# Kernel tuning notes

Measured on AMD Instinct MI355X. Metric: run time of the kernel, lower is better.

The kernel has to match this reference:

```python
import jax, jax.numpy as jnp
import numpy as np

D_MODEL = 128
N_HEADS = 8
HEAD_DIM = D_MODEL // N_HEADS
N_NODES = 50000
N_EDGES = 640000


def setup_inputs() -> dict:
    key = jax.random.key(0)
    ks = jax.random.split(key, 10)
    sd = 1.0 / np.sqrt(D_MODEL)
    return {
        "node_embeds": jax.random.normal(ks[0], (N_NODES, D_MODEL), dtype=jnp.float32),
        "edge_index": jax.random.randint(ks[1], (2, N_EDGES), 0, N_NODES, dtype=jnp.int64),
        "Wq": jax.random.uniform(ks[2], (D_MODEL, D_MODEL), jnp.float32, -sd, sd),
        "bq": jax.random.uniform(ks[3], (D_MODEL,), jnp.float32, -sd, sd),
        "Wk": jax.random.uniform(ks[4], (D_MODEL, D_MODEL), jnp.float32, -sd, sd),
        "bk": jax.random.uniform(ks[5], (D_MODEL,), jnp.float32, -sd, sd),
        "Wv": jax.random.uniform(ks[6], (D_MODEL, D_MODEL), jnp.float32, -sd, sd),
        "bv": jax.random.uniform(ks[7], (D_MODEL,), jnp.float32, -sd, sd),
        "gamma": jnp.ones((D_MODEL,), jnp.float32),
        "beta": jnp.zeros((D_MODEL,), jnp.float32),
    }


def reference(node_embeds, edge_index, Wq, bq, Wk, bk, Wv, bv, gamma, beta):
    num_nodes = node_embeds.shape[0]
    rows, cols = edge_index[0], edge_index[1]
    src = node_embeds[rows]  # (E, d)
    tgt = node_embeds[cols]  # (E, d)
    q = (src @ Wq.T + bq).reshape(-1, N_HEADS, HEAD_DIM)
    k = (tgt @ Wk.T + bk).reshape(-1, N_HEADS, HEAD_DIM)
    v = (tgt @ Wv.T + bv).reshape(-1, N_HEADS, HEAD_DIM)
    att = jnp.einsum('ehd,ehd->eh', q, k) / jnp.sqrt(jnp.float32(HEAD_DIM))
    exp_att = jnp.exp(jnp.clip(att, -10.0, 10.0))  # (E, h)
    att_sum = jax.ops.segment_sum(exp_att, rows, num_segments=num_nodes)  # (N, h)
    att_norm = exp_att / (att_sum[rows] + 1e-8)
    weighted_v = (att_norm[..., None] * v).reshape(-1, D_MODEL)  # (E, d)
    out = jax.ops.segment_sum(weighted_v, rows, num_segments=num_nodes)
    out = out + node_embeds
    # LayerNorm, eps=1e-6
    mu = jnp.mean(out, axis=-1, keepdims=True)
    var = jnp.mean(jnp.square(out - mu), axis=-1, keepdims=True)
    out = (out - mu) * jax.lax.rsqrt(var + 1e-6) * gamma + beta
    return out
```

## Files before the change

### kernel.cpp

```cpp
#include <hip/hip_runtime.h>
#include <hip/hip_bf16.h>
#include <cstdint>

#define D_MODEL 128
#define N_HEADS 8
#define HEAD_DIM 16

typedef __attribute__((ext_vector_type(8))) short bf16x8;
typedef __attribute__((ext_vector_type(4))) float f32x4;

static __device__ __forceinline__ float b2f(unsigned short u) {
  unsigned int x = ((unsigned int)u) << 16;
  return __builtin_bit_cast(float, x);
}
static __device__ __forceinline__ unsigned short f2b(float f) {
  __hip_bfloat16 h = __float2bfloat16(f);
  return __builtin_bit_cast(unsigned short, h);
}

__global__ __launch_bounds__(256) void hist_qkv_kernel(
    const int* __restrict__ rows, int* __restrict__ cnt, int E,
    const float* __restrict__ X,
    const float* __restrict__ Wq, const float* __restrict__ Wk,
    const float* __restrict__ Wv,
    const float* __restrict__ bq, const float* __restrict__ bk,
    const float* __restrict__ bv,
    unsigned short* __restrict__ Qo, unsigned short* __restrict__ Ko,
    unsigned short* __restrict__ Vo, int N, int nbQ)
{
  __shared__ unsigned short Wl[128 * 128];

  if ((int)blockIdx.x >= nbQ) {
    const int e = (blockIdx.x - nbQ) * 256 + threadIdx.x;
    if (e < E) atomicAdd(&cnt[rows[e]], 1);
    return;
  }

  const int t    = threadIdx.x;
  const int wave = t >> 6;
  const int l    = t & 63;
  const int lr   = l & 15;
  const int lg   = l >> 4;
  const int nw   = blockIdx.x * 128 + wave * 32;

  bf16x8 a[2][4];
  #pragma unroll
  for (int ng = 0; ng < 2; ++ng) {
    const int arow = nw + ng * 16 + lr;
    if (arow < N) {
      const float* xp = X + (size_t)arow * D_MODEL + lg * 8;
      #pragma unroll
      for (int ks = 0; ks < 4; ++ks) {
        const float4 f0 = reinterpret_cast<const float4*>(xp + ks * 32)[0];
        const float4 f1 = reinterpret_cast<const float4*>(xp + ks * 32)[1];
        unsigned short tm[8];
        tm[0] = f2b(f0.x); tm[1] = f2b(f0.y); tm[2] = f2b(f0.z); tm[3] = f2b(f0.w);
        tm[4] = f2b(f1.x); tm[5] = f2b(f1.y); tm[6] = f2b(f1.z); tm[7] = f2b(f1.w);
        a[ng][ks] = *reinterpret_cast<bf16x8*>(tm);
      }
    } else {
      #pragma unroll
      for (int ks = 0; ks < 4; ++ks) a[ng][ks] = bf16x8{0,0,0,0,0,0,0,0};
    }
  }

  const float* wmats[3]  = {Wq, Wk, Wv};
  const float* biases[3] = {bq, bk, bv};
  unsigned short* outs[3] = {Qo, Ko, Vo};

  #pragma unroll 1
  for (int m = 0; m < 3; ++m) {
    __syncthreads();
    {
      const float* __restrict__ wsrc = wmats[m];
      uint4* wl4 = reinterpret_cast<uint4*>(Wl);
      #pragma unroll
      for (int i = 0; i < 8; ++i) {
        const int cg = i * 256 + t;
        const int r  = cg >> 4;
        const int j  = cg & 15;
        const float4 f0 = reinterpret_cast<const float4*>(wsrc + cg * 8)[0];
        const float4 f1 = reinterpret_cast<const float4*>(wsrc + cg * 8)[1];
        unsigned short tm[8];
        tm[0] = f2b(f0.x); tm[1] = f2b(f0.y); tm[2] = f2b(f0.z); tm[3] = f2b(f0.w);
        tm[4] = f2b(f1.x); tm[5] = f2b(f1.y); tm[6] = f2b(f1.z); tm[7] = f2b(f1.w);
        wl4[r * 16 + (j ^ (r & 7))] = *reinterpret_cast<uint4*>(tm);
      }
    }
    __syncthreads();

    unsigned short* __restrict__ O = outs[m];
    const float* __restrict__ bias = biases[m];
    float bias8[8];
    #pragma unroll
    for (int c = 0; c < 8; ++c) bias8[c] = bias[c * 16 + lr];

    #pragma unroll
    for (int c = 0; c < 8; ++c) {
      const int row = c * 16 + lr;
      bf16x8 w[4];
      #pragma unroll
      for (int ks = 0; ks < 4; ++ks) {
        const int j = ks * 4 + lg;
        w[ks] = *reinterpret_cast<const bf16x8*>(
            Wl + ((row * 16 + (j ^ (row & 7))) * 8));
      }
      #pragma unroll
      for (int ng = 0; ng < 2; ++ng) {
        f32x4 acc = {bias8[c], bias8[c], bias8[c], bias8[c]};
        #pragma unroll
        for (int ks = 0; ks < 4; ++ks)
          acc = __builtin_amdgcn_mfma_f32_16x16x32_bf16(a[ng][ks], w[ks], acc, 0, 0, 0);
        #pragma unroll
        for (int r = 0; r < 4; ++r) {
          const int orow = nw + ng * 16 + lg * 4 + r;
          if (orow < N) O[(size_t)orow * D_MODEL + c * 16 + lr] = f2b(acc[r]);
        }
      }
    }
  }
}

__global__ __launch_bounds__(256) void emit_kernel(
    const int* __restrict__ cnt, int* __restrict__ row_ptr,
    int* __restrict__ row_cur, int N, int E)
{
  __shared__ int red[4];
  __shared__ int psum[256];
  __shared__ int base_s;
  const int b = blockIdx.x;
  const int t = threadIdx.x;

  int s = 0;
  {
    const int npre4 = (b * 1024) >> 2;
    const int4* c4 = reinterpret_cast<const int4*>(cnt);
    for (int i = t; i < npre4; i += 256) {
      const int4 v = c4[i];
      s += v.x + v.y + v.z + v.w;
    }
  }
  #pragma unroll
  for (int off = 32; off > 0; off >>= 1) s += __shfl_xor(s, off, 64);
  if ((t & 63) == 0) red[t >> 6] = s;
  __syncthreads();
  if (t == 0) base_s = red[0] + red[1] + red[2] + red[3];

  const int base = b * 1024 + t * 4;
  int v[4];
  #pragma unroll
  for (int i = 0; i < 4; ++i)
    v[i] = (base + i < N) ? cnt[base + i] : 0;
  const int local = v[0] + v[1] + v[2] + v[3];
  psum[t] = local;
  __syncthreads();
  for (int off = 1; off < 256; off <<= 1) {
    const int other = (t >= off) ? psum[t - off] : 0;
    __syncthreads();
    psum[t] += other;
    __syncthreads();
  }
  int pre = base_s + psum[t] - local;
  #pragma unroll
  for (int i = 0; i < 4; ++i) {
    const int idx = base + i;
    if (idx < N) {
      row_ptr[idx] = pre;
      row_cur[idx] = pre;
      pre += v[i];
    }
  }
  if (b == 0 && t == 0) row_ptr[N] = E;
}

__global__ __launch_bounds__(256) void scatter_kernel(
    const int* __restrict__ rows, const int* __restrict__ cols,
    int* __restrict__ row_cur, int* __restrict__ csr_cols, int E)
{
  const int e = blockIdx.x * 256 + threadIdx.x;
  if (e >= E) return;
  const int pos = atomicAdd(&row_cur[rows[e]], 1);
  csr_cols[pos] = cols[e];
}

__global__ __launch_bounds__(256) void fused_kernel(
    const unsigned short* __restrict__ Q, const unsigned short* __restrict__ K,
    const unsigned short* __restrict__ V, const float* __restrict__ X,
    const int* __restrict__ row_ptr, const int* __restrict__ csr_cols,
    const float* __restrict__ gamma, const float* __restrict__ beta,
    float* __restrict__ out, int N)
{
  __shared__ float lds[4][576];
  const int wv = threadIdx.x >> 6;
  const int n  = blockIdx.x * 4 + wv;
  if (n >= N) return;
  const int l  = threadIdx.x & 63;
  const int h  = l & 7;
  const int g  = l >> 3;
  const int hd = l >> 3;

  unsigned* __restrict__ Vu = reinterpret_cast<unsigned*>(lds[wv]);
  float*    __restrict__ El = lds[wv] + 512;

  float qf[16];
  {
    const unsigned short* qp = Q + (size_t)n * D_MODEL + h * HEAD_DIM;
    const bf16x8 q0 = *reinterpret_cast<const bf16x8*>(qp);
    const bf16x8 q1 = *reinterpret_cast<const bf16x8*>(qp + 8);
    #pragma unroll
    for (int i = 0; i < 8; ++i) {
      qf[i]     = b2f((unsigned short)q0[i]);
      qf[8 + i] = b2f((unsigned short)q1[i]);
    }
  }

  float accx = 0.f, accy = 0.f, dlane = 0.f;
  const int e0 = row_ptr[n];
  const int e1 = row_ptr[n + 1];

  const int rcol = (l & 7) * 64;
  const int rrot = (l >> 3) + 4 * (l & 7);

  for (int eb = e0; eb < e1; eb += 8) {
    const int  eg    = eb + g;
    const bool valid = eg < e1;
    const int  c     = valid ? csr_cols[eg] : 0;

    const unsigned short* kp = K + (size_t)c * D_MODEL + h * HEAD_DIM;
    const unsigned short* vp = V + (size_t)c * D_MODEL + h * HEAD_DIM;
    const bf16x8 k0 = *reinterpret_cast<const bf16x8*>(kp);
    const bf16x8 k1 = *reinterpret_cast<const bf16x8*>(kp + 8);
    const bf16x8 v0 = *reinterpret_cast<const bf16x8*>(vp);
    const bf16x8 v1 = *reinterpret_cast<const bf16x8*>(vp + 8);

    float s = 0.f;
    #pragma unroll
    for (int i = 0; i < 8; ++i) {
      s = fmaf(qf[i],     b2f((unsigned short)k0[i]), s);
      s = fmaf(qf[8 + i], b2f((unsigned short)k1[i]), s);
    }
    s *= 0.25f;
    s = fminf(fmaxf(s, -10.f), 10.f);
    const float ea = valid ? __expf(s) : 0.f;
    dlane += ea;

    El[l] = ea;
    {
      const uint4 u0 = __builtin_bit_cast(uint4, v0);
      const uint4 u1 = __builtin_bit_cast(uint4, v1);
      Vu[0 * 64 + ((l +  0) & 63)] = u0.x;
      Vu[1 * 64 + ((l +  4) & 63)] = u0.y;
      Vu[2 * 64 + ((l +  8) & 63)] = u0.z;
      Vu[3 * 64 + ((l + 12) & 63)] = u0.w;
      Vu[4 * 64 + ((l + 16) & 63)] = u1.x;
      Vu[5 * 64 + ((l + 20) & 63)] = u1.y;
      Vu[6 * 64 + ((l + 24) & 63)] = u1.z;
      Vu[7 * 64 + ((l + 28) & 63)] = u1.w;
    }
    __builtin_amdgcn_sched_barrier(0);

    #pragma unroll
    for (int j = 0; j < 8; ++j) {
      const float    aj = El[j * 8 + hd];
      const unsigned vv = Vu[rcol + ((j * 8 + rrot) & 63)];
      accx = fmaf(aj, b2f((unsigned short)(vv & 0xffffu)), accx);
      accy = fmaf(aj, b2f((unsigned short)(vv >> 16)), accy);
    }
    __builtin_amdgcn_sched_barrier(0);
  }

  dlane += __shfl_xor(dlane, 8,  64);
  dlane += __shfl_xor(dlane, 16, 64);
  dlane += __shfl_xor(dlane, 32, 64);
  const float denom = __shfl(dlane, hd, 64);

  const float inv = 1.f / (denom + 1e-8f);
  const float2 x = reinterpret_cast<const float2*>(X + (size_t)n * D_MODEL)[l];
  const float a0 = accx * inv + x.x;
  const float a1 = accy * inv + x.y;

  float sm = a0 + a1;
  float ss = a0 * a0 + a1 * a1;
  #pragma unroll
  for (int off = 32; off > 0; off >>= 1) {
    sm += __shfl_xor(sm, off, 64);
    ss += __shfl_xor(ss, off, 64);
  }
  const float mean = sm * (1.f / 128.f);
  const float var  = ss * (1.f / 128.f) - mean * mean;
  const float rs   = rsqrtf(var + 1e-6f);
  const float2 gm = reinterpret_cast<const float2*>(gamma)[l];
  const float2 bt = reinterpret_cast<const float2*>(beta)[l];
  float2 o;
  o.x = (a0 - mean) * rs * gm.x + bt.x;
  o.y = (a1 - mean) * rs * gm.y + bt.y;
  reinterpret_cast<float2*>(out + (size_t)n * D_MODEL)[l] = o;
}

extern "C" void kernel_launch(void* const* d_in, const int* in_sizes, int n_in,
                              void* d_out, int out_size, void* d_ws, size_t ws_size,
                              hipStream_t stream)
{
  const float* X     = (const float*)d_in[0];
  const int*   ei    = (const int*)  d_in[1];
  const float* Wq    = (const float*)d_in[2];
  const float* bq    = (const float*)d_in[3];
  const float* Wk    = (const float*)d_in[4];
  const float* bk    = (const float*)d_in[5];
  const float* Wv    = (const float*)d_in[6];
  const float* bv    = (const float*)d_in[7];
  const float* gamma = (const float*)d_in[8];
  const float* beta  = (const float*)d_in[9];

  const int N = in_sizes[0] / D_MODEL;
  const int E = in_sizes[1] / 2;
  const int* rows = ei;
  const int* cols = ei + E;

  const size_t nd = (size_t)N * D_MODEL;
  unsigned short* Qb = (unsigned short*)d_ws;
  unsigned short* Kb = Qb + nd;
  unsigned short* Vb = Kb + nd;
  int* row_cnt  = (int*)(Vb + nd);
  int* row_ptr  = row_cnt + N;
  int* row_cur  = row_ptr + N + 1;
  int* csr_cols = row_cur + N;

  const int nb  = (N + 1023) / 1024;
  const int nbE = (E + 255) / 256;
  const int nbQ = (N + 127) / 128;

  hipMemsetAsync(row_cnt, 0, (size_t)N * sizeof(int), stream);

  hist_qkv_kernel<<<nbQ + nbE, 256, 0, stream>>>(
      rows, row_cnt, E, X, Wq, Wk, Wv, bq, bk, bv, Qb, Kb, Vb, N, nbQ);

  emit_kernel<<<nb, 256, 0, stream>>>(row_cnt, row_ptr, row_cur, N, E);

  scatter_kernel<<<nbE, 256, 0, stream>>>(rows, cols, row_cur, csr_cols, E);

  fused_kernel<<<(N + 3) / 4, 256, 0, stream>>>(
      Qb, Kb, Vb, X, row_ptr, csr_cols, gamma, beta, (float*)d_out, N);
}
```

Baseline: 149.3 us.

## Pre-convert weights to bf16 and co-schedule QKV GEMM with CSR scatter

The weight fp32→bf16 conversion moves out of every GEMM block into a small prepass, and that prepass shares a launch with the histogram. The QKV projection blocks now run in the same launch as the CSR scatter instead of alongside the histogram. Each GEMM block loads ready-made bf16 weights into LDS, which removes the per-block conversion work and halves the weight bytes read. The aim is to balance the short emit and scatter stages against the GEMM so that more of the pipeline overlaps, at the cost of a small extra workspace buffer.

```diff
diff --git a/kernel.cpp b/kernel.cpp
--- a/kernel.cpp
+++ b/kernel.cpp
@@ -18,11 +18,85 @@
   return __builtin_bit_cast(unsigned short, h);
 }
 
-__global__ __launch_bounds__(256) void hist_qkv_kernel(
+__global__ __launch_bounds__(256) void hist_cvtw_kernel(
     const int* __restrict__ rows, int* __restrict__ cnt, int E,
-    const float* __restrict__ X,
     const float* __restrict__ Wq, const float* __restrict__ Wk,
-    const float* __restrict__ Wv,
+    const float* __restrict__ Wv, unsigned short* __restrict__ Wb)
+{
+  if (blockIdx.x < 24) {
+    const int wb = blockIdx.x;
+    const int m  = wb >> 3;
+    const float* src = (m == 0) ? Wq : (m == 1) ? Wk : Wv;
+    unsigned short* dst = Wb + (size_t)m * 16384;
+    const int base = ((wb & 7) * 256 + threadIdx.x) * 8;
+    const float4 a = reinterpret_cast<const float4*>(src + base)[0];
+    const float4 c = reinterpret_cast<const float4*>(src + base)[1];
+    unsigned short tmp[8];
+    tmp[0] = f2b(a.x); tmp[1] = f2b(a.y); tmp[2] = f2b(a.z); tmp[3] = f2b(a.w);
+    tmp[4] = f2b(c.x); tmp[5] = f2b(c.y); tmp[6] = f2b(c.z); tmp[7] = f2b(c.w);
+    reinterpret_cast<uint4*>(dst + base)[0] = *reinterpret_cast<uint4*>(tmp);
+  } else {
+    const int e = (blockIdx.x - 24) * 256 + threadIdx.x;
+    if (e < E) atomicAdd(&cnt[rows[e]], 1);
+  }
+}
+
+__global__ __launch_bounds__(256) void emit_kernel(
+    const int* __restrict__ cnt, int* __restrict__ row_ptr,
+    int* __restrict__ row_cur, int N, int E)
+{
+  __shared__ int red[4];
+  __shared__ int psum[256];
+  __shared__ int base_s;
+  const int b = blockIdx.x;
+  const int t = threadIdx.x;
+
+  int s = 0;
+  {
+    const int npre4 = (b * 1024) >> 2;
+    const int4* c4 = reinterpret_cast<const int4*>(cnt);
+    for (int i = t; i < npre4; i += 256) {
+      const int4 v = c4[i];
+      s += v.x + v.y + v.z + v.w;
+    }
+  }
+  #pragma unroll
+  for (int off = 32; off > 0; off >>= 1) s += __shfl_xor(s, off, 64);
+  if ((t & 63) == 0) red[t >> 6] = s;
+  __syncthreads();
+  if (t == 0) base_s = red[0] + red[1] + red[2] + red[3];
+
+  const int base = b * 1024 + t * 4;
+  int v[4];
+  #pragma unroll
+  for (int i = 0; i < 4; ++i)
+    v[i] = (base + i < N) ? cnt[base + i] : 0;
+  const int local = v[0] + v[1] + v[2] + v[3];
+  psum[t] = local;
+  __syncthreads();
+  for (int off = 1; off < 256; off <<= 1) {
+    const int other = (t >= off) ? psum[t - off] : 0;
+    __syncthreads();
+    psum[t] += other;
+    __syncthreads();
+  }
+  int pre = base_s + psum[t] - local;
+  #pragma unroll
+  for (int i = 0; i < 4; ++i) {
+    const int idx = base + i;
+    if (idx < N) {
+      row_ptr[idx] = pre;
+      row_cur[idx] = pre;
+      pre += v[i];
+    }
+  }
+  if (b == 0 && t == 0) row_ptr[N] = E;
+}
+
+__global__ __launch_bounds__(256) void scatter_qkv_kernel(
+    const int* __restrict__ rows, const int* __restrict__ cols,
+    int* __restrict__ row_cur, int* __restrict__ csr_cols, int E,
+    const float* __restrict__ X, const unsigned short* __restrict__ Wb,
     const float* __restrict__ bq, const float* __restrict__ bk,
     const float* __restrict__ bv,
     unsigned short* __restrict__ Qo, unsigned short* __restrict__ Ko,
@@ -32,7 +106,10 @@
 
   if ((int)blockIdx.x >= nbQ) {
     const int e = (blockIdx.x - nbQ) * 256 + threadIdx.x;
-    if (e < E) atomicAdd(&cnt[rows[e]], 1);
+    if (e < E) {
+      const int pos = atomicAdd(&row_cur[rows[e]], 1);
+      csr_cols[pos] = cols[e];
+    }
     return;
   }
 
@@ -64,7 +141,6 @@
     }
   }
 
-  const float* wmats[3]  = {Wq, Wk, Wv};
   const float* biases[3] = {bq, bk, bv};
   unsigned short* outs[3] = {Qo, Ko, Vo};
 
@@ -72,19 +148,14 @@
   for (int m = 0; m < 3; ++m) {
     __syncthreads();
     {
-      const float* __restrict__ wsrc = wmats[m];
+      const uint4* wsrc = reinterpret_cast<const uint4*>(Wb + (size_t)m * 16384);
       uint4* wl4 = reinterpret_cast<uint4*>(Wl);
       #pragma unroll
       for (int i = 0; i < 8; ++i) {
         const int cg = i * 256 + t;
         const int r  = cg >> 4;
         const int j  = cg & 15;
-        const float4 f0 = reinterpret_cast<const float4*>(wsrc + cg * 8)[0];
-        const float4 f1 = reinterpret_cast<const float4*>(wsrc + cg * 8)[1];
-        unsigned short tm[8];
-        tm[0] = f2b(f0.x); tm[1] = f2b(f0.y); tm[2] = f2b(f0.z); tm[3] = f2b(f0.w);
-        tm[4] = f2b(f1.x); tm[5] = f2b(f1.y); tm[6] = f2b(f1.z); tm[7] = f2b(f1.w);
-        wl4[r * 16 + (j ^ (r & 7))] = *reinterpret_cast<uint4*>(tm);
+        wl4[r * 16 + (j ^ (r & 7))] = wsrc[cg];
       }
     }
     __syncthreads();
@@ -119,68 +190,6 @@
       }
     }
   }
-}
-
-__global__ __launch_bounds__(256) void emit_kernel(
-    const int* __restrict__ cnt, int* __restrict__ row_ptr,
-    int* __restrict__ row_cur, int N, int E)
-{
-  __shared__ int red[4];
-  __shared__ int psum[256];
-  __shared__ int base_s;
-  const int b = blockIdx.x;
-  const int t = threadIdx.x;
-
-  int s = 0;
-  {
-    const int npre4 = (b * 1024) >> 2;
-    const int4* c4 = reinterpret_cast<const int4*>(cnt);
-    for (int i = t; i < npre4; i += 256) {
-      const int4 v = c4[i];
-      s += v.x + v.y + v.z + v.w;
-    }
-  }
-  #pragma unroll
-  for (int off = 32; off > 0; off >>= 1) s += __shfl_xor(s, off, 64);
-  if ((t & 63) == 0) red[t >> 6] = s;
-  __syncthreads();
-  if (t == 0) base_s = red[0] + red[1] + red[2] + red[3];
-
-  const int base = b * 1024 + t * 4;
-  int v[4];
-  #pragma unroll
-  for (int i = 0; i < 4; ++i)
-    v[i] = (base + i < N) ? cnt[base + i] : 0;
-  const int local = v[0] + v[1] + v[2] + v[3];
-  psum[t] = local;
-  __syncthreads();
-  for (int off = 1; off < 256; off <<= 1) {
-    const int other = (t >= off) ? psum[t - off] : 0;
-    __syncthreads();
-    psum[t] += other;
-    __syncthreads();
-  }
-  int pre = base_s + psum[t] - local;
-  #pragma unroll
-  for (int i = 0; i < 4; ++i) {
-    const int idx = base + i;
-    if (idx < N) {
-      row_ptr[idx] = pre;
-      row_cur[idx] = pre;
-      pre += v[i];
-    }
-  }
-  if (b == 0 && t == 0) row_ptr[N] = E;
-}
-
-__global__ __launch_bounds__(256) void scatter_kernel(
-    const int* __restrict__ rows, const int* __restrict__ cols,
-    int* __restrict__ row_cur, int* __restrict__ csr_cols, int E)
-{
-  const int e = blockIdx.x * 256 + threadIdx.x;
-  if (e >= E) return;
-  const int pos = atomicAdd(&row_cur[rows[e]], 1);
-  csr_cols[pos] = cols[e];
 }
 
 __global__ __launch_bounds__(256) void fused_kernel(
@@ -318,7 +327,8 @@
   const int* cols = ei + E;
 
   const size_t nd = (size_t)N * D_MODEL;
-  unsigned short* Qb = (unsigned short*)d_ws;
+  unsigned short* Wb = (unsigned short*)d_ws;
+  unsigned short* Qb = Wb + 3 * 16384;
   unsigned short* Kb = Qb + nd;
   unsigned short* Vb = Kb + nd;
   int* row_cnt  = (int*)(Vb + nd);
@@ -332,12 +342,14 @@
 
   hipMemsetAsync(row_cnt, 0, (size_t)N * sizeof(int), stream);
 
-  hist_qkv_kernel<<<nbQ + nbE, 256, 0, stream>>>(
-      rows, row_cnt, E, X, Wq, Wk, Wv, bq, bk, bv, Qb, Kb, Vb, N, nbQ);
+  hist_cvtw_kernel<<<24 + nbE, 256, 0, stream>>>(
+      rows, row_cnt, E, Wq, Wk, Wv, Wb);
 
   emit_kernel<<<nb, 256, 0, stream>>>(row_cnt, row_ptr, row_cur, N, E);
 
-  scatter_kernel<<<nbE, 256, 0, stream>>>(rows, cols, row_cur, csr_cols, E);
+  scatter_qkv_kernel<<<nbQ + nbE, 256, 0, stream>>>(
+      rows, cols, row_cur, csr_cols, E,
+      X, Wb, bq, bk, bv, Qb, Kb, Vb, N, nbQ);
 
   fused_kernel<<<(N + 3) / 4, 256, 0, stream>>>(
       Qb, Kb, Vb, X, row_ptr, csr_cols, gamma, beta, (float*)d_out, N);
```

Measured after the change: 147.5 us. About the same (-1.2%).
